# Kernel tuning notes

Measured on AMD Instinct MI355X. Metric: run time of the kernel, lower is better.

The kernel has to match this reference:

```python
import jax, jax.numpy as jnp
import numpy as np


def setup_inputs() -> dict:
    key = jax.random.key(0)
    k1, k2 = jax.random.split(key)
    B, F, L = 2048, 1, 512       # batch, n_features, seq_len
    N = 100000                   # fitted training windows
    x_enc = jax.random.normal(k1, (B, F, L), dtype=jnp.float32)
    X_fit = jax.random.normal(k2, (N, F * L), dtype=jnp.float32)
    return {"x_enc": x_enc, "X_fit": X_fit, "n_neighbors": 5}


def reference(x_enc, X_fit, n_neighbors):
    # x_enc: [B, F, L]; X_fit: [N, F*L]
    B, F, L = x_enc.shape
    q = x_enc.reshape(B, -1)                       # [B, D]
    # Squared Euclidean distances: ||q||^2 + ||x||^2 - 2 q.x^T  -> [B, N]
    q_sq = jnp.sum(q * q, axis=-1, keepdims=True)           # [B, 1]
    x_sq = jnp.sum(X_fit * X_fit, axis=-1)[None, :]         # [1, N]
    d2 = q_sq + x_sq - 2.0 * jnp.einsum("bd,nd->bn", q, X_fit)
    # k nearest = k smallest distances
    _, idx = jax.lax.top_k(-d2, n_neighbors)                # idx: [B, k]
    neigh = X_fit[idx]                                      # [B, k, D]
    y_hat = jnp.mean(neigh, axis=1).reshape(B, F, L)        # neighbor mean
    return y_hat
```

## Files before the change

### kernel.cpp

```cpp
#include <hip/hip_runtime.h>
#include <float.h>

#define D 512
#define BM 128
#define BN 256
#define BK 32
#define NCH 64
#define MPC 8
#define TR 16
#define SCS 148

typedef __attribute__((ext_vector_type(8))) short short8;
typedef __attribute__((ext_vector_type(4))) float f32x4;
typedef const __attribute__((address_space(1))) void gv_t;
typedef __attribute__((address_space(3))) void lv_t;

__device__ __forceinline__ void gl2lds16(const void* g, void* l) {
    __builtin_amdgcn_global_load_lds((gv_t*)g, (lv_t*)l, 16, 0, 0);
}

__device__ __forceinline__ unsigned short f2bf(float f) {
    unsigned u = __float_as_uint(f);
    return (unsigned short)((u + 0x7FFF + ((u >> 16) & 1)) >> 16);
}

template <int K>
__device__ __forceinline__ void insertK(float* bs, int* bi, float v, int id) {
    if (v < bs[K - 1]) {
        bs[K - 1] = v; bi[K - 1] = id;
#pragma unroll
        for (int r = K - 1; r >= 1; --r) {
            if (bs[r] < bs[r - 1]) {
                float tf = bs[r]; bs[r] = bs[r - 1]; bs[r - 1] = tf;
                int ti = bi[r]; bi[r] = bi[r - 1]; bi[r - 1] = ti;
            }
        }
    }
}

__global__ void convert_x(const float* __restrict__ X, unsigned short* __restrict__ Xbf,
                          float* __restrict__ xsq, int N, int padN) {
    int row = blockIdx.x * 4 + (threadIdx.x >> 6);
    int lane = threadIdx.x & 63;
    if (row >= padN) return;
    unsigned short ob[8];
    float s = 0.0f;
    if (row < N) {
        const float* p = X + (size_t)row * D + lane * 8;
        float4 a = *(const float4*)p;
        float4 b = *(const float4*)(p + 4);
        s = a.x * a.x + a.y * a.y + a.z * a.z + a.w * a.w
          + b.x * b.x + b.y * b.y + b.z * b.z + b.w * b.w;
        ob[0] = f2bf(a.x); ob[1] = f2bf(a.y); ob[2] = f2bf(a.z); ob[3] = f2bf(a.w);
        ob[4] = f2bf(b.x); ob[5] = f2bf(b.y); ob[6] = f2bf(b.z); ob[7] = f2bf(b.w);
    } else {
#pragma unroll
        for (int i = 0; i < 8; ++i) ob[i] = 0;
    }
    *(uint4*)(Xbf + (size_t)row * D + lane * 8) = *(uint4*)ob;
#pragma unroll
    for (int off = 32; off > 0; off >>= 1) s += __shfl_down(s, off, 64);
    if (lane == 0) xsq[row] = (row < N) ? s : 1e30f;
}

__global__ void convert_q(const float* __restrict__ Q, unsigned short* __restrict__ Qbf) {
    int row = blockIdx.x * 4 + (threadIdx.x >> 6);
    int lane = threadIdx.x & 63;
    const float* p = Q + (size_t)row * D + lane * 8;
    float4 a = *(const float4*)p;
    float4 b = *(const float4*)(p + 4);
    unsigned short ob[8];
    ob[0] = f2bf(-2.0f * a.x); ob[1] = f2bf(-2.0f * a.y);
    ob[2] = f2bf(-2.0f * a.z); ob[3] = f2bf(-2.0f * a.w);
    ob[4] = f2bf(-2.0f * b.x); ob[5] = f2bf(-2.0f * b.y);
    ob[6] = f2bf(-2.0f * b.z); ob[7] = f2bf(-2.0f * b.w);
    *(uint4*)(Qbf + (size_t)row * D + lane * 8) = *(uint4*)ob;
}

__global__ __launch_bounds__(256, 2) void score_mfma(
    const unsigned short* __restrict__ Qbf,
    const unsigned short* __restrict__ Xbf,
    const float* __restrict__ xsq,
    float* __restrict__ candS, int* __restrict__ candI,
    int ntiles)
{
    __shared__ union {
        struct { unsigned short A[BM * BK]; unsigned short B[BN * BK]; } st;
        float sc[64 * SCS];
        struct { float ms[256][MPC]; int mi[256][MPC]; } mg;
    } u;

    const int tid = threadIdx.x;
    const int wave = tid >> 6;
    const int lane = tid & 63;
    const int quad = lane >> 4;
    const int l15 = lane & 15;
    const int wm = wave & 1;
    const int wn = wave >> 1;
    const int qt = blockIdx.x;
    const int chunk = blockIdx.y;

    const int m_scan = tid >> 1;
    const int h_scan = tid & 1;

    float ts[MPC]; int ti8[MPC];
#pragma unroll
    for (int r = 0; r < MPC; ++r) { ts[r] = FLT_MAX; ti8[r] = -1; }

    const int srow = tid >> 2;
    const int sseg = (((tid & 3) ^ ((tid >> 3) & 3)) * 8);
    const int kxor = ((quad ^ ((l15 >> 1) & 3)) * 8);

    for (int tile = chunk; tile < ntiles; tile += NCH) {
        const int n0 = tile * BN;

        f32x4 acc[4][8];
#pragma unroll
        for (int tj = 0; tj < 8; ++tj) {
            float v = xsq[n0 + wn * 128 + tj * 16 + l15];
            f32x4 vv = {v, v, v, v};
#pragma unroll
            for (int ti = 0; ti < 4; ++ti) acc[ti][tj] = vv;
        }

        for (int k0 = 0; k0 < D; k0 += BK) {
            __syncthreads();
            gl2lds16(Qbf + ((size_t)(qt * BM + srow) * D + k0 + sseg),
                     u.st.A + (size_t)(wave * 64) * 8);
            gl2lds16(Qbf + ((size_t)(qt * BM + 64 + srow) * D + k0 + sseg),
                     u.st.A + (size_t)(256 + wave * 64) * 8);
#pragma unroll
            for (int c = 0; c < 4; ++c)
                gl2lds16(Xbf + ((size_t)(n0 + c * 64 + srow) * D + k0 + sseg),
                         u.st.B + (size_t)(c * 256 + wave * 64) * 8);
            __syncthreads();

            short8 af[4], bf[8];
#pragma unroll
            for (int ti = 0; ti < 4; ++ti)
                af[ti] = *(const short8*)&u.st.A[(wm * 64 + ti * 16 + l15) * BK + kxor];
#pragma unroll
            for (int tj = 0; tj < 8; ++tj)
                bf[tj] = *(const short8*)&u.st.B[(wn * 128 + tj * 16 + l15) * BK + kxor];
#pragma unroll
            for (int ti = 0; ti < 4; ++ti)
#pragma unroll
                for (int tj = 0; tj < 8; ++tj)
                    acc[ti][tj] = __builtin_amdgcn_mfma_f32_16x16x32_bf16(
                        af[ti], bf[tj], acc[ti][tj], 0, 0, 0);
        }

#pragma unroll
        for (int g = 0; g < 4; ++g) {
            __syncthreads();
            if (wn == (g >> 1)) {
#pragma unroll
                for (int ti = 0; ti < 4; ++ti)
#pragma unroll
                    for (int jj = 0; jj < 4; ++jj)
                        *(f32x4*)&u.sc[(jj * 16 + l15) * SCS + wm * 64 + ti * 16 + quad * 4] =
                            acc[ti][(g & 1) * 4 + jj];
            }
            __syncthreads();
#pragma unroll 8
            for (int i = 0; i < 32; ++i) {
                int n_loc = h_scan * 32 + i;
                float s = u.sc[n_loc * SCS + m_scan];
                insertK<MPC>(ts, ti8, s, n0 + g * 64 + n_loc);
            }
        }
    }

    __syncthreads();
#pragma unroll
    for (int r = 0; r < MPC; ++r) { u.mg.ms[tid][r] = ts[r]; u.mg.mi[tid][r] = ti8[r]; }
    __syncthreads();
    if (h_scan == 0) {
#pragma unroll
        for (int r = 0; r < MPC; ++r)
            insertK<MPC>(ts, ti8, u.mg.ms[tid + 1][r], u.mg.mi[tid + 1][r]);
        size_t base = ((size_t)(qt * BM + m_scan) * NCH + chunk) * MPC;
#pragma unroll
        for (int r = 0; r < MPC; ++r) { candS[base + r] = ts[r]; candI[base + r] = ti8[r]; }
    }
}

__global__ void rescore_kernel(const float* __restrict__ Q, const float* __restrict__ X,
                               const float* __restrict__ xsq,
                               const float* __restrict__ candS, const int* __restrict__ candI,
                               float* __restrict__ out) {
    const int b = blockIdx.x;
    const int tid = threadIdx.x;
    const int wave = tid >> 6;
    const int lane = tid & 63;
    __shared__ int exI[TR];
    __shared__ float exS[TR];
    __shared__ int top5[5];

    if (wave == 0) {
        const float* cs = candS + (size_t)b * NCH * MPC;
        const int* ci = candI + (size_t)b * NCH * MPC;
        int h = 0;
        float cur = cs[lane * MPC];
        for (int r = 0; r < TR; ++r) {
            float v = cur; int wl = lane;
#pragma unroll
            for (int off = 1; off < 64; off <<= 1) {
                float ov = __shfl_xor(v, off, 64);
                int owl = __shfl_xor(wl, off, 64);
                if (ov < v || (ov == v && owl < wl)) { v = ov; wl = owl; }
            }
            if (lane == wl) {
                exI[r] = ci[lane * MPC + h];
                ++h;
                cur = (h < MPC) ? cs[lane * MPC + h] : FLT_MAX;
            }
        }
    }
    __syncthreads();

    const float* qr = Q + (size_t)b * D;
#pragma unroll
    for (int cc = 0; cc < 4; ++cc) {
        int c = wave * 4 + cc;
        int idx = exI[c];
        const float* xr = X + (size_t)idx * D;
        float4 qa = *(const float4*)(qr + lane * 8);
        float4 qb = *(const float4*)(qr + lane * 8 + 4);
        float4 xa = *(const float4*)(xr + lane * 8);
        float4 xb = *(const float4*)(xr + lane * 8 + 4);
        float p = qa.x * xa.x + qa.y * xa.y + qa.z * xa.z + qa.w * xa.w
                + qb.x * xb.x + qb.y * xb.y + qb.z * xb.z + qb.w * xb.w;
#pragma unroll
        for (int off = 32; off > 0; off >>= 1) p += __shfl_down(p, off, 64);
        if (lane == 0) exS[c] = xsq[idx] - 2.0f * p;
    }
    __syncthreads();

    if (tid == 0) {
        float fs[5]; int fi[5];
#pragma unroll
        for (int r = 0; r < 5; ++r) { fs[r] = FLT_MAX; fi[r] = -1; }
        for (int i = 0; i < TR; ++i) insertK<5>(fs, fi, exS[i], exI[i]);
#pragma unroll
        for (int r = 0; r < 5; ++r) top5[r] = fi[r];
    }
    __syncthreads();

#pragma unroll
    for (int dd = 0; dd < 2; ++dd) {
        int d = tid + dd * 256;
        float s = 0.0f;
#pragma unroll
        for (int r = 0; r < 5; ++r) s += X[(size_t)top5[r] * D + d];
        out[(size_t)b * D + d] = s / 5.0f;
    }
}

extern "C" void kernel_launch(void* const* d_in, const int* in_sizes, int n_in,
                              void* d_out, int out_size, void* d_ws, size_t ws_size,
                              hipStream_t stream) {
    const float* x_enc = (const float*)d_in[0];
    const float* X_fit = (const float*)d_in[1];
    float* out = (float*)d_out;
    const int B = in_sizes[0] / D;
    const int N = in_sizes[1] / D;
    const int padN = ((N + BN - 1) / BN) * BN;
    const int ntiles = padN / BN;
    const int qtiles = B / BM;

    char* w = (char*)d_ws;
    unsigned short* Xbf = (unsigned short*)w;            w += (size_t)padN * D * 2;
    unsigned short* Qbf = (unsigned short*)w;            w += (size_t)B * D * 2;
    float* xsq = (float*)w;                              w += (size_t)padN * 4;
    float* candS = (float*)w;                            w += (size_t)B * NCH * MPC * 4;
    int* candI = (int*)w;

    hipLaunchKernelGGL(convert_x, dim3(padN / 4), dim3(256), 0, stream, X_fit, Xbf, xsq, N, padN);
    hipLaunchKernelGGL(convert_q, dim3(B / 4), dim3(256), 0, stream, x_enc, Qbf);
    hipLaunchKernelGGL(score_mfma, dim3(qtiles, NCH), dim3(256), 0, stream,
                       Qbf, Xbf, xsq, candS, candI, ntiles);
    hipLaunchKernelGGL(rescore_kernel, dim3(B), dim3(256), 0, stream,
                       x_enc, X_fit, xsq, candS, candI, out);
}
```

Baseline: 891.8 us.

## Double-buffer LDS K-tiles with prefetch and per-wave top-k scan

Adds a two-stage LDS buffer for the bf16 GEMM in the scoring kernel, issuing the next K slice (and the first slice of the next N tile) before computing the current one, with explicit vmcnt waits and raw s_barrier in place of two __syncthreads per step. The epilogue now has each wave write its own 16x64 score patch to a private XOR-swizzled LDS region and scan it with per-lane top-8 insertion, avoiding block-wide barriers between score groups. The cross-wave merge is restructured to match. This costs twice the staging LDS and relies on hand-counted vmcnt values being right.

```diff
diff --git a/kernel.cpp b/kernel.cpp
--- a/kernel.cpp
+++ b/kernel.cpp
@@ -8,7 +8,6 @@
 #define NCH 64
 #define MPC 8
 #define TR 16
-#define SCS 148
 
 typedef __attribute__((ext_vector_type(8))) short short8;
 typedef __attribute__((ext_vector_type(4))) float f32x4;
@@ -77,6 +76,46 @@
     *(uint4*)(Qbf + (size_t)row * D + lane * 8) = *(uint4*)ob;
 }
 
+struct KBuf { unsigned short A[BM * BK]; unsigned short B[BN * BK]; };
+
+#define STAGE(buf, nn0, kk0)                                                        \
+    do {                                                                            \
+        const size_t kof_ = (size_t)(kk0) + sseg;                                   \
+        gl2lds16(Qbf + (size_t)(qrow0 + srow) * D + kof_, (buf)->A + wave * 512);   \
+        gl2lds16(Qbf + (size_t)(qrow0 + 64 + srow) * D + kof_,                      \
+                 (buf)->A + 2048 + wave * 512);                                     \
+        gl2lds16(Xbf + (size_t)((nn0) + srow) * D + kof_, (buf)->B + wave * 512);   \
+        gl2lds16(Xbf + (size_t)((nn0) + 64 + srow) * D + kof_,                      \
+                 (buf)->B + 2048 + wave * 512);                                     \
+        gl2lds16(Xbf + (size_t)((nn0) + 128 + srow) * D + kof_,                     \
+                 (buf)->B + 4096 + wave * 512);                                     \
+        gl2lds16(Xbf + (size_t)((nn0) + 192 + srow) * D + kof_,                     \
+                 (buf)->B + 6144 + wave * 512);                                     \
+    } while (0)
+
+#define COMPUTE(CUR)                                                                 \
+    do {                                                                             \
+        const KBuf* cb_ = &s.st[CUR];                                                \
+        short8 af_[4], bf_[8];                                                       \
+        _Pragma("unroll") for (int ti = 0; ti < 4; ++ti)                             \
+            af_[ti] = *(const short8*)&cb_->A[(wm * 64 + ti * 16 + l15) * BK + kxor];\
+        _Pragma("unroll") for (int tj = 0; tj < 8; ++tj)                             \
+            bf_[tj] = *(const short8*)&cb_->B[(wn * 128 + tj * 16 + l15) * BK + kxor];\
+        _Pragma("unroll") for (int ti = 0; ti < 4; ++ti)                             \
+            _Pragma("unroll") for (int tj = 0; tj < 8; ++tj)                         \
+                acc[ti][tj] = __builtin_amdgcn_mfma_f32_16x16x32_bf16(               \
+                    af_[ti], bf_[tj], acc[ti][tj], 0, 0, 0);                         \
+    } while (0)
+
+#define KITER(CUR, NXT, NK0, WTOK)                                  \
+    do {                                                            \
+        __builtin_amdgcn_s_barrier();                               \
+        STAGE(&s.st[NXT], n0, (NK0));                               \
+        asm volatile("s_waitcnt vmcnt(" #WTOK ")" ::: "memory");    \
+        __builtin_amdgcn_s_barrier();                               \
+        COMPUTE(CUR);                                               \
+    } while (0)
+
 __global__ __launch_bounds__(256, 2) void score_mfma(
     const unsigned short* __restrict__ Qbf,
     const unsigned short* __restrict__ Xbf,
@@ -84,11 +123,13 @@
     float* __restrict__ candS, int* __restrict__ candI,
     int ntiles)
 {
-    __shared__ union {
-        struct { unsigned short A[BM * BK]; unsigned short B[BN * BK]; } st;
-        float sc[64 * SCS];
-        struct { float ms[256][MPC]; int mi[256][MPC]; } mg;
-    } u;
+    __shared__ struct {
+        KBuf st[2];
+        union {
+            float scw[4][16 * 64];
+            struct { float ms[4][64][MPC]; int mi[4][64][MPC]; } mg;
+        } u2;
+    } s;
 
     const int tid = threadIdx.x;
     const int wave = tid >> 6;
@@ -99,87 +140,80 @@
     const int wn = wave >> 1;
     const int qt = blockIdx.x;
     const int chunk = blockIdx.y;
-
-    const int m_scan = tid >> 1;
-    const int h_scan = tid & 1;
-
-    float ts[MPC]; int ti8[MPC];
-#pragma unroll
-    for (int r = 0; r < MPC; ++r) { ts[r] = FLT_MAX; ti8[r] = -1; }
+    const int qrow0 = qt * BM;
 
     const int srow = tid >> 2;
     const int sseg = (((tid & 3) ^ ((tid >> 3) & 3)) * 8);
     const int kxor = ((quad ^ ((l15 >> 1) & 3)) * 8);
+    const int xsw = (l15 & 7) << 2;
+
+    float ts[MPC]; int ti8[MPC];
+#pragma unroll
+    for (int r = 0; r < MPC; ++r) { ts[r] = FLT_MAX; ti8[r] = -1; }
+
+    float* scw = s.u2.scw[wave];
+
+    STAGE(&s.st[0], chunk * BN, 0);
 
     for (int tile = chunk; tile < ntiles; tile += NCH) {
         const int n0 = tile * BN;
+        const bool last = (tile + NCH) >= ntiles;
 
         f32x4 acc[4][8];
 #pragma unroll
+        for (int ti = 0; ti < 4; ++ti)
+#pragma unroll
+            for (int tj = 0; tj < 8; ++tj) acc[ti][tj] = (f32x4){0.f, 0.f, 0.f, 0.f};
+
+        float xv[8];
+#pragma unroll
+        for (int tj = 0; tj < 8; ++tj) xv[tj] = xsq[n0 + wn * 128 + tj * 16 + l15];
+
+        KITER(0, 1, BK, 14);
+        for (int kk = 0; kk < 6; ++kk) {
+            const int kb = kk * 2;
+            KITER(1, 0, (kb + 2) * BK, 6);
+            KITER(0, 1, (kb + 3) * BK, 6);
+        }
+        KITER(1, 0, 14 * BK, 6);
+        KITER(0, 1, 15 * BK, 6);
+        __builtin_amdgcn_s_barrier();
+        if (!last) {
+            STAGE(&s.st[0], n0 + NCH * BN, 0);
+            asm volatile("s_waitcnt vmcnt(6)" ::: "memory");
+        } else {
+            asm volatile("s_waitcnt vmcnt(0)" ::: "memory");
+        }
+        __builtin_amdgcn_s_barrier();
+        COMPUTE(1);
+
+#pragma unroll
         for (int tj = 0; tj < 8; ++tj) {
-            float v = xsq[n0 + wn * 128 + tj * 16 + l15];
-            f32x4 vv = {v, v, v, v};
-#pragma unroll
-            for (int ti = 0; ti < 4; ++ti) acc[ti][tj] = vv;
-        }
-
-        for (int k0 = 0; k0 < D; k0 += BK) {
-            __syncthreads();
-            gl2lds16(Qbf + ((size_t)(qt * BM + srow) * D + k0 + sseg),
-                     u.st.A + (size_t)(wave * 64) * 8);
-            gl2lds16(Qbf + ((size_t)(qt * BM + 64 + srow) * D + k0 + sseg),
-                     u.st.A + (size_t)(256 + wave * 64) * 8);
-#pragma unroll
-            for (int c = 0; c < 4; ++c)
-                gl2lds16(Xbf + ((size_t)(n0 + c * 64 + srow) * D + k0 + sseg),
-                         u.st.B + (size_t)(c * 256 + wave * 64) * 8);
-            __syncthreads();
-
-            short8 af[4], bf[8];
-#pragma unroll
-            for (int ti = 0; ti < 4; ++ti)
-                af[ti] = *(const short8*)&u.st.A[(wm * 64 + ti * 16 + l15) * BK + kxor];
-#pragma unroll
-            for (int tj = 0; tj < 8; ++tj)
-                bf[tj] = *(const short8*)&u.st.B[(wn * 128 + tj * 16 + l15) * BK + kxor];
-#pragma unroll
-            for (int ti = 0; ti < 4; ++ti)
-#pragma unroll
-                for (int tj = 0; tj < 8; ++tj)
-                    acc[ti][tj] = __builtin_amdgcn_mfma_f32_16x16x32_bf16(
-                        af[ti], bf[tj], acc[ti][tj], 0, 0, 0);
-        }
-
-#pragma unroll
-        for (int g = 0; g < 4; ++g) {
-            __syncthreads();
-            if (wn == (g >> 1)) {
-#pragma unroll
-                for (int ti = 0; ti < 4; ++ti)
-#pragma unroll
-                    for (int jj = 0; jj < 4; ++jj)
-                        *(f32x4*)&u.sc[(jj * 16 + l15) * SCS + wm * 64 + ti * 16 + quad * 4] =
-                            acc[ti][(g & 1) * 4 + jj];
-            }
-            __syncthreads();
-#pragma unroll 8
-            for (int i = 0; i < 32; ++i) {
-                int n_loc = h_scan * 32 + i;
-                float s = u.sc[n_loc * SCS + m_scan];
-                insertK<MPC>(ts, ti8, s, n0 + g * 64 + n_loc);
-            }
-        }
-    }
-
-    __syncthreads();
-#pragma unroll
-    for (int r = 0; r < MPC; ++r) { u.mg.ms[tid][r] = ts[r]; u.mg.mi[tid][r] = ti8[r]; }
-    __syncthreads();
-    if (h_scan == 0) {
+            const float xvt = xv[tj];
+#pragma unroll
+            for (int ti = 0; ti < 4; ++ti) {
+                f32x4 a = acc[ti][tj];
+                a.x += xvt; a.y += xvt; a.z += xvt; a.w += xvt;
+                *(f32x4*)&scw[l15 * 64 + ((ti * 16 + quad * 4) ^ xsw)] = a;
+            }
+            const int cb0 = n0 + wn * 128 + tj * 16;
+#pragma unroll 4
+            for (int n = 0; n < 16; ++n) {
+                float v = scw[n * 64 + (lane ^ ((n & 7) << 2))];
+                insertK<MPC>(ts, ti8, v, cb0 + n);
+            }
+        }
+    }
+
+    __syncthreads();
+#pragma unroll
+    for (int r = 0; r < MPC; ++r) { s.u2.mg.ms[wave][lane][r] = ts[r]; s.u2.mg.mi[wave][lane][r] = ti8[r]; }
+    __syncthreads();
+    if (wn == 0) {
 #pragma unroll
         for (int r = 0; r < MPC; ++r)
-            insertK<MPC>(ts, ti8, u.mg.ms[tid + 1][r], u.mg.mi[tid + 1][r]);
-        size_t base = ((size_t)(qt * BM + m_scan) * NCH + chunk) * MPC;
+            insertK<MPC>(ts, ti8, s.u2.mg.ms[wave + 2][lane][r], s.u2.mg.mi[wave + 2][lane][r]);
+        size_t base = ((size_t)(qrow0 + wm * 64 + lane) * NCH + chunk) * MPC;
 #pragma unroll
         for (int r = 0; r < MPC; ++r) { candS[base + r] = ts[r]; candI[base + r] = ti8[r]; }
     }
@@ -250,10 +284,10 @@
 #pragma unroll
     for (int dd = 0; dd < 2; ++dd) {
         int d = tid + dd * 256;
-        float s = 0.0f;
-#pragma unroll
-        for (int r = 0; r < 5; ++r) s += X[(size_t)top5[r] * D + d];
-        out[(size_t)b * D + d] = s / 5.0f;
+        float sacc = 0.0f;
+#pragma unroll
+        for (int r = 0; r < 5; ++r) sacc += X[(size_t)top5[r] * D + d];
+        out[(size_t)b * D + d] = sacc / 5.0f;
     }
 }
 
```

Result: slower. 1.188 ms (+33.2%).
